# Kernel optimization log

Hardware: AMD Instinct MI355X
Metric: run time of the kernel (lower is better)

The kernel has to match this reference:

```python
import jax, jax.numpy as jnp
import numpy as np

D_MODEL = 1024
N_HEAD = 16
D_K = D_MODEL // N_HEAD
B, T = 4, 2048


def setup_inputs() -> dict:
    key = jax.random.key(0)
    ks = jax.random.split(key, 12)
    s = 1.0 / np.sqrt(D_MODEL)
    inp = {
        "q": jax.random.normal(ks[0], (B, T, D_MODEL), jnp.float32),
        "k": jax.random.normal(ks[1], (B, T, D_MODEL), jnp.float32),
        "v": jax.random.normal(ks[2], (B, T, D_MODEL), jnp.float32),
        # causal mask: True = allowed
        "mask": jnp.tril(jnp.ones((T, T), bool))[None, None, :, :],
        "w_q": jax.random.uniform(ks[3], (D_MODEL, D_MODEL), jnp.float32, -s, s),
        "b_q": jax.random.uniform(ks[4], (D_MODEL,), jnp.float32, -s, s),
        "w_k": jax.random.uniform(ks[5], (D_MODEL, D_MODEL), jnp.float32, -s, s),
        "b_k": jax.random.uniform(ks[6], (D_MODEL,), jnp.float32, -s, s),
        "w_v": jax.random.uniform(ks[7], (D_MODEL, D_MODEL), jnp.float32, -s, s),
        "b_v": jax.random.uniform(ks[8], (D_MODEL,), jnp.float32, -s, s),
        "w_o": jax.random.uniform(ks[9], (D_MODEL, D_MODEL), jnp.float32, -s, s),
        "b_o": jax.random.uniform(ks[10], (D_MODEL,), jnp.float32, -s, s),
    }
    return inp


def reference(q, k, v, mask, w_q, b_q, w_k, b_k, w_v, b_v, w_o, b_o):
    b, tq, d = q.shape
    tk = k.shape[1]
    # projections (torch Linear: x @ W^T + b)
    qh = (q @ w_q.T + b_q).reshape(b, tq, N_HEAD, D_K).transpose(0, 2, 1, 3)
    kh = (k @ w_k.T + b_k).reshape(b, tk, N_HEAD, D_K).transpose(0, 2, 1, 3)
    vh = (v @ w_v.T + b_v).reshape(b, tk, N_HEAD, D_K).transpose(0, 2, 1, 3)
    # scores: (b, h, tq, tk)
    scores = jnp.einsum("bhqd,bhkd->bhqk", qh, kh) / jnp.sqrt(jnp.float32(D_K))
    scores = jnp.where(mask, scores, jnp.finfo(scores.dtype).min)
    attn = jax.nn.softmax(scores, axis=-1)
    out = jnp.einsum("bhqk,bhkd->bhqd", attn, vh)
    out = out.transpose(0, 2, 1, 3).reshape(b, tq, d)
    return out @ w_o.T + b_o
```

## Files before the change

### kernel.cpp

```cpp
#include <hip/hip_runtime.h>

typedef unsigned short u16;
typedef __attribute__((ext_vector_type(8))) short bf16x8;
typedef __attribute__((ext_vector_type(4))) float f32x4;

#define D_MODEL 1024
#define T_SEQ   2048
#define NB      4
#define NH      16
#define DKH     64

__device__ __forceinline__ u16 f2bf(float x) {
  union { float f; unsigned u; } v; v.f = x;
  unsigned r = v.u + 0x7fffu + ((v.u >> 16) & 1u);
  return (u16)(r >> 16);
}
__device__ __forceinline__ unsigned pack2(float a, float b) {
  return (unsigned)f2bf(a) | ((unsigned)f2bf(b) << 16);
}
__device__ __forceinline__ float fexp2(float x) {
#if __has_builtin(__builtin_amdgcn_exp2f)
  return __builtin_amdgcn_exp2f(x);
#else
  return __expf(x * 0.6931471805599453f);
#endif
}

__device__ __forceinline__ void gload16(const void* g, void* l) {
  __builtin_amdgcn_global_load_lds(
      (const __attribute__((address_space(1))) unsigned*)g,
      (__attribute__((address_space(3))) unsigned*)l, 16, 0, 0);
}

__global__ void cast_w4(const float* __restrict__ s0, const float* __restrict__ s1,
                        const float* __restrict__ s2, const float* __restrict__ s3,
                        u16* __restrict__ o0, u16* __restrict__ o1,
                        u16* __restrict__ o2, u16* __restrict__ o3) {
  const int which = blockIdx.y;
  const float* s = which == 0 ? s0 : which == 1 ? s1 : which == 2 ? s2 : s3;
  u16* o = which == 0 ? o0 : which == 1 ? o1 : which == 2 ? o2 : o3;
  int i = ((int)blockIdx.x * 256 + (int)threadIdx.x) * 4;
  float4 v = *(const float4*)(s + i);
  uint2 u; u.x = pack2(v.x, v.y); u.y = pack2(v.z, v.w);
  *(uint2*)(o + i) = u;
}

__global__ __launch_bounds__(256) void gemm_qkv(
    const float* __restrict__ qin, const float* __restrict__ kin, const float* __restrict__ vin,
    const u16* __restrict__ wq, const u16* __restrict__ wk, const u16* __restrict__ wv,
    const float* __restrict__ bqp, const float* __restrict__ bkp, const float* __restrict__ bvp,
    u16* __restrict__ Xq, u16* __restrict__ Xk, u16* __restrict__ Xv) {
  const int z = blockIdx.z;
  const float* A = z == 0 ? qin : z == 1 ? kin : vin;
  const u16* W = z == 0 ? wq : z == 1 ? wk : wv;
  const float* bias = z == 0 ? bqp : z == 1 ? bkp : bvp;
  u16* C = z == 0 ? Xq : z == 1 ? Xk : Xv;
  const float osc = z == 0 ? 0.18033688011112042f : 1.0f;
  const int K = 1024, N = 1024;

  __shared__ __align__(16) u16 As[128 * 72];
  __shared__ __align__(16) u16 Bs[128 * 64];
  const int tid = threadIdx.x;
  const int w = tid >> 6, lane = tid & 63;
  const int wm = w & 1, wn = w >> 1;
  const int l15 = lane & 15, quad = lane >> 4;
  const int m0 = blockIdx.x * 128, n0 = blockIdx.y * 128;
  const int srow = tid >> 3;
  const int scol = (tid & 7) * 8;
  const int lrow = lane >> 3;
  const int lcol = ((lane & 7) ^ lrow) * 8;

  const u16* gB = W + (size_t)(n0 + w * 32 + lrow) * K + lcol;
  u16* lB = Bs + w * 32 * 64;

  f32x4 zero4 = {0.f, 0.f, 0.f, 0.f};
  f32x4 acc[4][4];
#pragma unroll
  for (int i = 0; i < 4; ++i)
#pragma unroll
    for (int j = 0; j < 4; ++j) acc[i][j] = zero4;

  for (int kb = 0; kb < K; kb += 64) {
    uint4 ra[4];
#pragma unroll
    for (int r = 0; r < 4; ++r) {
      const float* p = A + (size_t)(m0 + r * 32 + srow) * K + kb + scol;
      float4 x = *(const float4*)p;
      float4 y = *(const float4*)(p + 4);
      ra[r].x = pack2(x.x, x.y); ra[r].y = pack2(x.z, x.w);
      ra[r].z = pack2(y.x, y.y); ra[r].w = pack2(y.z, y.w);
    }
    __syncthreads();
#pragma unroll
    for (int t = 0; t < 4; ++t) gload16(gB + kb + t * 8 * K, lB + t * 512);
#pragma unroll
    for (int r = 0; r < 4; ++r)
      *(uint4*)(As + (r * 32 + srow) * 72 + scol) = ra[r];
    __syncthreads();

#pragma unroll
    for (int ks = 0; ks < 2; ++ks) {
      const int sB = (((ks * 4 + quad) ^ (l15 & 7)) * 8);
      bf16x8 af[4], bfr[4];
#pragma unroll
      for (int i = 0; i < 4; ++i)
        af[i] = *(const bf16x8*)(As + (wm * 64 + i * 16 + l15) * 72 + ks * 32 + quad * 8);
#pragma unroll
      for (int i = 0; i < 4; ++i)
        bfr[i] = *(const bf16x8*)(Bs + (wn * 64 + i * 16 + l15) * 64 + sB);
#pragma unroll
      for (int mi = 0; mi < 4; ++mi)
#pragma unroll
        for (int ni = 0; ni < 4; ++ni)
          acc[mi][ni] = __builtin_amdgcn_mfma_f32_16x16x32_bf16(af[mi], bfr[ni], acc[mi][ni], 0, 0, 0);
    }
  }

#pragma unroll
  for (int ni = 0; ni < 4; ++ni) {
    int col = n0 + wn * 64 + ni * 16 + l15;
    float bv = bias[col];
#pragma unroll
    for (int mi = 0; mi < 4; ++mi) {
      int row = m0 + wm * 64 + mi * 16 + quad * 4;
#pragma unroll
      for (int r = 0; r < 4; ++r)
        C[(size_t)(row + r) * N + col] = f2bf((acc[mi][ni][r] + bv) * osc);
    }
  }
}

__global__ __launch_bounds__(256) void gemm_nt_f32out(const u16* __restrict__ Ab,
                                                      const u16* __restrict__ W,
                                                      const float* __restrict__ bias,
                                                      float* __restrict__ Cp,
                                                      int M, int N, int K) {
  __shared__ __align__(16) u16 As[128 * 64];
  __shared__ __align__(16) u16 Bs[128 * 64];
  const int tid = threadIdx.x;
  const int w = tid >> 6, lane = tid & 63;
  const int wm = w & 1, wn = w >> 1;
  const int l15 = lane & 15, quad = lane >> 4;
  const int m0 = blockIdx.x * 128, n0 = blockIdx.y * 128;
  const int lrow = lane >> 3;
  const int lcol = ((lane & 7) ^ lrow) * 8;

  const u16* gA = Ab + (size_t)(m0 + w * 32 + lrow) * K + lcol;
  const u16* gB = W  + (size_t)(n0 + w * 32 + lrow) * K + lcol;
  u16* lA = As + w * 32 * 64;
  u16* lB = Bs + w * 32 * 64;

  f32x4 zero4 = {0.f, 0.f, 0.f, 0.f};
  f32x4 acc[4][4];
#pragma unroll
  for (int i = 0; i < 4; ++i)
#pragma unroll
    for (int j = 0; j < 4; ++j) acc[i][j] = zero4;

  for (int kb = 0; kb < K; kb += 64) {
    __syncthreads();
#pragma unroll
    for (int t = 0; t < 4; ++t) gload16(gA + kb + t * 8 * K, lA + t * 512);
#pragma unroll
    for (int t = 0; t < 4; ++t) gload16(gB + kb + t * 8 * K, lB + t * 512);
    __syncthreads();

#pragma unroll
    for (int ks = 0; ks < 2; ++ks) {
      const int sA = (((ks * 4 + quad) ^ (l15 & 7)) * 8);
      bf16x8 af[4], bfr[4];
#pragma unroll
      for (int i = 0; i < 4; ++i)
        af[i] = *(const bf16x8*)(As + (wm * 64 + i * 16 + l15) * 64 + sA);
#pragma unroll
      for (int i = 0; i < 4; ++i)
        bfr[i] = *(const bf16x8*)(Bs + (wn * 64 + i * 16 + l15) * 64 + sA);
#pragma unroll
      for (int mi = 0; mi < 4; ++mi)
#pragma unroll
        for (int ni = 0; ni < 4; ++ni)
          acc[mi][ni] = __builtin_amdgcn_mfma_f32_16x16x32_bf16(af[mi], bfr[ni], acc[mi][ni], 0, 0, 0);
    }
  }

#pragma unroll
  for (int ni = 0; ni < 4; ++ni) {
    int col = n0 + wn * 64 + ni * 16 + l15;
    float bv = bias[col];
#pragma unroll
    for (int mi = 0; mi < 4; ++mi) {
      int row = m0 + wm * 64 + mi * 16 + quad * 4;
#pragma unroll
      for (int r = 0; r < 4; ++r)
        Cp[(size_t)(row + r) * N + col] = acc[mi][ni][r] + bv;
    }
  }
}

__global__ __launch_bounds__(256) void attn_fwd(const u16* __restrict__ Xq,
                                                const u16* __restrict__ Xk,
                                                const u16* __restrict__ Xv,
                                                u16* __restrict__ O) {
  __shared__ __align__(16) u16 Kt[2][64 * 64];
  __shared__ __align__(16) u16 Vt[2][64 * 72];

  const int qt = 15 - (int)blockIdx.x;
  const int h = blockIdx.y, b = blockIdx.z;
  const int tid = threadIdx.x;
  const int w = tid >> 6, lane = tid & 63;
  const int l15 = lane & 15, quad = lane >> 4;
  const size_t base = (size_t)b * T_SEQ * D_MODEL;
  const int hd = h * DKH;
  const int q0 = qt * 128;
  const int rowb0 = q0 + w * 32;

  const int krow = lane >> 3;
  const int kcol = ((lane & 7) ^ krow) * 8;
  const u16* gK = Xk + base + (size_t)(w * 16 + krow) * D_MODEL + hd + kcol;

  const int vkey = lane, vdp = w;
  const int skey = (vkey & 0x20) | ((vkey & 0xC) << 1) | ((vkey & 0x10) >> 2) | (vkey & 3);
  const u16* gV = Xv + base + (size_t)vkey * D_MODEL + hd + vdp * 16;

  bf16x8 bq[2][2];
#pragma unroll
  for (int mi = 0; mi < 2; ++mi)
#pragma unroll
    for (int ks = 0; ks < 2; ++ks)
      bq[mi][ks] = *(const bf16x8*)(Xq + base + (size_t)(rowb0 + mi * 16 + l15) * D_MODEL
                                    + hd + ks * 32 + quad * 8);

  bf16x8 bones;
#pragma unroll
  for (int i = 0; i < 8; ++i) bones[i] = (short)0x3F80;

  f32x4 zero4 = {0.f, 0.f, 0.f, 0.f};
  f32x4 o[4][2], ol[2];
#pragma unroll
  for (int di = 0; di < 4; ++di)
#pragma unroll
    for (int mi = 0; mi < 2; ++mi) o[di][mi] = zero4;
#pragma unroll
  for (int mi = 0; mi < 2; ++mi) ol[mi] = zero4;

  const int nkt = 2 * qt + 2;

  gload16(gK, Kt[0] + (w * 16) * 64);
  gload16(gK + (size_t)8 * D_MODEL, Kt[0] + (w * 16 + 8) * 64);
  uint4 va0 = *(const uint4*)gV;
  uint4 va1 = *(const uint4*)(gV + 8);

  for (int kt = 0; kt < nkt; ++kt) {
    const int k0 = kt * 64;
    const int buf = kt & 1;

    {
      union { uint4 u; u16 hh[8]; } u0, u1;
      u0.u = va0; u1.u = va1;
      u16* vtb = Vt[buf];
#pragma unroll
      for (int i = 0; i < 8; ++i) {
        vtb[(vdp * 16 + i) * 72 + skey] = u0.hh[i];
        vtb[(vdp * 16 + 8 + i) * 72 + skey] = u1.hh[i];
      }
    }
    __syncthreads();

    if (kt + 1 < nkt) {
      const u16* gk2 = gK + (size_t)(k0 + 64) * D_MODEL;
      gload16(gk2, Kt[1 - buf] + (w * 16) * 64);
      gload16(gk2 + (size_t)8 * D_MODEL, Kt[1 - buf] + (w * 16 + 8) * 64);
      const u16* gv2 = gV + (size_t)(k0 + 64) * D_MODEL;
      va0 = *(const uint4*)gv2;
      va1 = *(const uint4*)(gv2 + 8);
    }

    f32x4 st[4][2];
#pragma unroll
    for (int ni = 0; ni < 4; ++ni) {
      const u16* kr = Kt[buf] + (ni * 16 + l15) * 64;
      bf16x8 a0 = *(const bf16x8*)(kr + ((quad ^ (l15 & 7)) * 8));
      bf16x8 a1 = *(const bf16x8*)(kr + (((4 + quad) ^ (l15 & 7)) * 8));
#pragma unroll
      for (int mi = 0; mi < 2; ++mi) {
        f32x4 t = zero4;
        t = __builtin_amdgcn_mfma_f32_16x16x32_bf16(a0, bq[mi][0], t, 0, 0, 0);
        t = __builtin_amdgcn_mfma_f32_16x16x32_bf16(a1, bq[mi][1], t, 0, 0, 0);
        st[ni][mi] = t;
      }
    }

    bf16x8 bp[2][2];
#pragma unroll
    for (int mi = 0; mi < 2; ++mi) {
      const int qa = rowb0 + mi * 16 + l15;
      if (k0 + 63 > rowb0 + mi * 16) {
#pragma unroll
        for (int ni = 0; ni < 4; ++ni)
#pragma unroll
          for (int r = 0; r < 4; ++r)
            if (k0 + ni * 16 + quad * 4 + r > qa) st[ni][mi][r] = -1e30f;
      }
      float p[4][4];
#pragma unroll
      for (int ni = 0; ni < 4; ++ni)
#pragma unroll
        for (int r = 0; r < 4; ++r)
          p[ni][r] = fexp2(st[ni][mi][r]);
#pragma unroll
      for (int js = 0; js < 2; ++js) {
        union { bf16x8 v; unsigned d[4]; } ub;
        ub.d[0] = pack2(p[2 * js][0], p[2 * js][1]);
        ub.d[1] = pack2(p[2 * js][2], p[2 * js][3]);
        ub.d[2] = pack2(p[2 * js + 1][0], p[2 * js + 1][1]);
        ub.d[3] = pack2(p[2 * js + 1][2], p[2 * js + 1][3]);
        bp[mi][js] = ub.v;
      }
    }

#pragma unroll
    for (int js = 0; js < 2; ++js) {
      bf16x8 av[4];
#pragma unroll
      for (int di = 0; di < 4; ++di)
        av[di] = *(const bf16x8*)(Vt[buf] + (di * 16 + l15) * 72 + js * 32 + quad * 8);
#pragma unroll
      for (int di = 0; di < 4; ++di)
#pragma unroll
        for (int mi = 0; mi < 2; ++mi)
          o[di][mi] = __builtin_amdgcn_mfma_f32_16x16x32_bf16(av[di], bp[mi][js], o[di][mi], 0, 0, 0);
#pragma unroll
      for (int mi = 0; mi < 2; ++mi)
        ol[mi] = __builtin_amdgcn_mfma_f32_16x16x32_bf16(bones, bp[mi][js], ol[mi], 0, 0, 0);
    }
  }

#pragma unroll
  for (int mi = 0; mi < 2; ++mi) {
    const float inv = 1.0f / ol[mi][0];
    const size_t qa = rowb0 + mi * 16 + l15;
#pragma unroll
    for (int di = 0; di < 4; ++di) {
      uint2 s2;
      s2.x = pack2(o[di][mi][0] * inv, o[di][mi][1] * inv);
      s2.y = pack2(o[di][mi][2] * inv, o[di][mi][3] * inv);
      *(uint2*)(O + base + qa * D_MODEL + hd + di * 16 + quad * 4) = s2;
    }
  }
}

extern "C" void kernel_launch(void* const* d_in, const int* in_sizes, int n_in,
                              void* d_out, int out_size, void* d_ws, size_t ws_size,
                              hipStream_t stream) {
  const float* q   = (const float*)d_in[0];
  const float* k   = (const float*)d_in[1];
  const float* v   = (const float*)d_in[2];
  const float* w_q = (const float*)d_in[4];  const float* b_q = (const float*)d_in[5];
  const float* w_k = (const float*)d_in[6];  const float* b_k = (const float*)d_in[7];
  const float* w_v = (const float*)d_in[8];  const float* b_v = (const float*)d_in[9];
  const float* w_o = (const float*)d_in[10]; const float* b_o = (const float*)d_in[11];

  u16* ws = (u16*)d_ws;
  const size_t NTD = (size_t)NB * T_SEQ * D_MODEL;
  const size_t WSZ = (size_t)D_MODEL * D_MODEL;
  u16* wqb = ws;
  u16* wkb = wqb + WSZ;
  u16* wvb = wkb + WSZ;
  u16* wob = wvb + WSZ;
  u16* Xq  = wob + WSZ;
  u16* Xk  = Xq + NTD;
  u16* Xv  = Xk + NTD;
  u16* Ob  = Xv + NTD;

  cast_w4<<<dim3(WSZ / 1024, 4), 256, 0, stream>>>(w_q, w_k, w_v, w_o, wqb, wkb, wvb, wob);

  gemm_qkv<<<dim3(64, 8, 3), 256, 0, stream>>>(q, k, v, wqb, wkb, wvb,
                                               b_q, b_k, b_v, Xq, Xk, Xv);

  attn_fwd<<<dim3(16, NH, NB), 256, 0, stream>>>(Xq, Xk, Xv, Ob);

  gemm_nt_f32out<<<dim3(64, 8), 256, 0, stream>>>(Ob, wob, b_o, (float*)d_out,
                                                  8192, 1024, 1024);
}
```

Measured before the change: 395.6 us.

## Pair causal query tiles per block, split keys across two wave halves, remap GEMM tiles

The attention kernel now runs 512 threads per block. Each block handles two query tiles (qt and 15-qt) so the causal work per block is balanced. The two 4-wave halves process the even and odd key tiles and merge their partial outputs and row sums through shared memory. V is stored in shared memory with an XOR swizzle instead of padding. The GEMMs use a 1D grid with an XCD-aware block-to-tile mapping meant to improve L2 locality, at the cost of extra synchronisation and shared-memory traffic in the merge.

```diff
diff --git a/kernel.cpp b/kernel.cpp
--- a/kernel.cpp
+++ b/kernel.cpp
@@ -43,6 +43,11 @@
   float4 v = *(const float4*)(s + i);
   uint2 u; u.x = pack2(v.x, v.y); u.y = pack2(v.z, v.w);
   *(uint2*)(o + i) = u;
+}
+
+__device__ __forceinline__ void xcd_decode(int bid, int& m0, int& n0) {
+  m0 = ((bid & 7) + ((bid >> 6) << 3)) << 7;
+  n0 = ((bid >> 3) & 7) << 7;
 }
 
 __global__ __launch_bounds__(256) void gemm_qkv(
@@ -64,7 +69,7 @@
   const int w = tid >> 6, lane = tid & 63;
   const int wm = w & 1, wn = w >> 1;
   const int l15 = lane & 15, quad = lane >> 4;
-  const int m0 = blockIdx.x * 128, n0 = blockIdx.y * 128;
+  int m0, n0; xcd_decode(blockIdx.x, m0, n0);
   const int srow = tid >> 3;
   const int scol = (tid & 7) * 8;
   const int lrow = lane >> 3;
@@ -141,7 +146,7 @@
   const int w = tid >> 6, lane = tid & 63;
   const int wm = w & 1, wn = w >> 1;
   const int l15 = lane & 15, quad = lane >> 4;
-  const int m0 = blockIdx.x * 128, n0 = blockIdx.y * 128;
+  int m0, n0; xcd_decode(blockIdx.x, m0, n0);
   const int lrow = lane >> 3;
   const int lcol = ((lane & 7) ^ lrow) * 8;
 
@@ -197,155 +202,210 @@
   }
 }
 
-__global__ __launch_bounds__(256) void attn_fwd(const u16* __restrict__ Xq,
-                                                const u16* __restrict__ Xk,
-                                                const u16* __restrict__ Xv,
-                                                u16* __restrict__ O) {
-  __shared__ __align__(16) u16 Kt[2][64 * 64];
-  __shared__ __align__(16) u16 Vt[2][64 * 72];
-
-  const int qt = 15 - (int)blockIdx.x;
+__global__ __launch_bounds__(512, 4) void attn_fwd(const u16* __restrict__ Xq,
+                                                   const u16* __restrict__ Xk,
+                                                   const u16* __restrict__ Xv,
+                                                   u16* __restrict__ O) {
+  __shared__ __align__(16) char smem[65536];
+
+  const int xp = blockIdx.x;
   const int h = blockIdx.y, b = blockIdx.z;
   const int tid = threadIdx.x;
   const int w = tid >> 6, lane = tid & 63;
+  const int half = w >> 2, wl = w & 3;
   const int l15 = lane & 15, quad = lane >> 4;
   const size_t base = (size_t)b * T_SEQ * D_MODEL;
   const int hd = h * DKH;
-  const int q0 = qt * 128;
-  const int rowb0 = q0 + w * 32;
+
+  u16* KtH = (u16*)(smem + half * 32768);
+  u16* VtH = (u16*)(smem + half * 32768 + 16384);
+  float* ML = (float*)(smem + 16384);
+  float* MO = (float*)(smem + 32768);
 
   const int krow = lane >> 3;
   const int kcol = ((lane & 7) ^ krow) * 8;
-  const u16* gK = Xk + base + (size_t)(w * 16 + krow) * D_MODEL + hd + kcol;
-
-  const int vkey = lane, vdp = w;
+  const u16* gK = Xk + base + (size_t)(wl * 16 + krow) * D_MODEL + hd + kcol;
+  const int vkey = lane;
   const int skey = (vkey & 0x20) | ((vkey & 0xC) << 1) | ((vkey & 0x10) >> 2) | (vkey & 3);
-  const u16* gV = Xv + base + (size_t)vkey * D_MODEL + hd + vdp * 16;
-
-  bf16x8 bq[2][2];
-#pragma unroll
-  for (int mi = 0; mi < 2; ++mi)
-#pragma unroll
-    for (int ks = 0; ks < 2; ++ks)
-      bq[mi][ks] = *(const bf16x8*)(Xq + base + (size_t)(rowb0 + mi * 16 + l15) * D_MODEL
-                                    + hd + ks * 32 + quad * 8);
+  const int scb = skey >> 3, sci = skey & 7;
+  const u16* gV = Xv + base + (size_t)vkey * D_MODEL + hd + wl * 16;
 
   bf16x8 bones;
 #pragma unroll
   for (int i = 0; i < 8; ++i) bones[i] = (short)0x3F80;
 
   f32x4 zero4 = {0.f, 0.f, 0.f, 0.f};
-  f32x4 o[4][2], ol[2];
-#pragma unroll
-  for (int di = 0; di < 4; ++di)
-#pragma unroll
-    for (int mi = 0; mi < 2; ++mi) o[di][mi] = zero4;
-#pragma unroll
-  for (int mi = 0; mi < 2; ++mi) ol[mi] = zero4;
-
-  const int nkt = 2 * qt + 2;
-
-  gload16(gK, Kt[0] + (w * 16) * 64);
-  gload16(gK + (size_t)8 * D_MODEL, Kt[0] + (w * 16 + 8) * 64);
-  uint4 va0 = *(const uint4*)gV;
-  uint4 va1 = *(const uint4*)(gV + 8);
-
-  for (int kt = 0; kt < nkt; ++kt) {
-    const int k0 = kt * 64;
-    const int buf = kt & 1;
-
-    {
-      union { uint4 u; u16 hh[8]; } u0, u1;
-      u0.u = va0; u1.u = va1;
-      u16* vtb = Vt[buf];
-#pragma unroll
-      for (int i = 0; i < 8; ++i) {
-        vtb[(vdp * 16 + i) * 72 + skey] = u0.hh[i];
-        vtb[(vdp * 16 + 8 + i) * 72 + skey] = u1.hh[i];
-      }
-    }
-    __syncthreads();
-
-    if (kt + 1 < nkt) {
-      const u16* gk2 = gK + (size_t)(k0 + 64) * D_MODEL;
-      gload16(gk2, Kt[1 - buf] + (w * 16) * 64);
-      gload16(gk2 + (size_t)8 * D_MODEL, Kt[1 - buf] + (w * 16 + 8) * 64);
-      const u16* gv2 = gV + (size_t)(k0 + 64) * D_MODEL;
-      va0 = *(const uint4*)gv2;
-      va1 = *(const uint4*)(gv2 + 8);
-    }
-
-    f32x4 st[4][2];
-#pragma unroll
-    for (int ni = 0; ni < 4; ++ni) {
-      const u16* kr = Kt[buf] + (ni * 16 + l15) * 64;
-      bf16x8 a0 = *(const bf16x8*)(kr + ((quad ^ (l15 & 7)) * 8));
-      bf16x8 a1 = *(const bf16x8*)(kr + (((4 + quad) ^ (l15 & 7)) * 8));
+  int tcnt = 0;
+
+  {
+    const u16* gk0 = gK + (size_t)(half * 64) * D_MODEL;
+    gload16(gk0, KtH + (wl * 16) * 64);
+    gload16(gk0 + (size_t)8 * D_MODEL, KtH + (wl * 16 + 8) * 64);
+  }
+  const u16* gv0 = gV + (size_t)(half * 64) * D_MODEL;
+  uint4 va0 = *(const uint4*)gv0;
+  uint4 va1 = *(const uint4*)(gv0 + 8);
+
+  for (int ph = 0; ph < 2; ++ph) {
+    const int qt = ph ? xp : 15 - xp;
+    const int q0 = qt << 7;
+    const int rowb0 = q0 + wl * 32;
+
+    bf16x8 bq[2][2];
+#pragma unroll
+    for (int mi = 0; mi < 2; ++mi)
+#pragma unroll
+      for (int ks = 0; ks < 2; ++ks)
+        bq[mi][ks] = *(const bf16x8*)(Xq + base + (size_t)(rowb0 + mi * 16 + l15) * D_MODEL
+                                      + hd + ks * 32 + quad * 8);
+
+    f32x4 o[4][2], ol[2];
+#pragma unroll
+    for (int di = 0; di < 4; ++di)
+#pragma unroll
+      for (int mi = 0; mi < 2; ++mi) o[di][mi] = zero4;
+#pragma unroll
+    for (int mi = 0; mi < 2; ++mi) ol[mi] = zero4;
+
+    const int cnt = qt + 1;
+
+    if (ph == 1 && half == 1) {
+      const int fb = tcnt & 1;
+      const u16* gk1 = gK + (size_t)64 * D_MODEL;
+      gload16(gk1, KtH + fb * 4096 + (wl * 16) * 64);
+      gload16(gk1 + (size_t)8 * D_MODEL, KtH + fb * 4096 + (wl * 16 + 8) * 64);
+    }
+
+    for (int i = 0; i < cnt; ++i, ++tcnt) {
+      const int k0 = (half + 2 * i) * 64;
+      const int buf = tcnt & 1;
+      u16* ktb = KtH + buf * 4096;
+      u16* vtb = VtH + buf * 4096;
+
+      {
+        union { uint4 u; u16 hh[8]; } u0, u1;
+        u0.u = va0; u1.u = va1;
+#pragma unroll
+        for (int ii = 0; ii < 8; ++ii) {
+          vtb[(wl * 16 + ii) * 64 + ((scb ^ ii) << 3) + sci] = u0.hh[ii];
+          vtb[(wl * 16 + 8 + ii) * 64 + ((scb ^ ii) << 3) + sci] = u1.hh[ii];
+        }
+      }
+      __syncthreads();
+
+      const bool inph = (i + 1 < cnt);
+      if (inph || ph == 0) {
+        const int k0n = inph ? k0 + 128 : half * 64;
+        if (inph || half == 0) {
+          const u16* gk2 = gK + (size_t)k0n * D_MODEL;
+          u16* ktn = KtH + (1 - buf) * 4096;
+          gload16(gk2, ktn + (wl * 16) * 64);
+          gload16(gk2 + (size_t)8 * D_MODEL, ktn + (wl * 16 + 8) * 64);
+        }
+        const u16* gv2 = gV + (size_t)k0n * D_MODEL;
+        va0 = *(const uint4*)gv2;
+        va1 = *(const uint4*)(gv2 + 8);
+      }
+
+      f32x4 st[4][2];
+#pragma unroll
+      for (int ni = 0; ni < 4; ++ni) {
+        const u16* kr = ktb + (ni * 16 + l15) * 64;
+        bf16x8 a0 = *(const bf16x8*)(kr + ((quad ^ (l15 & 7)) << 3));
+        bf16x8 a1 = *(const bf16x8*)(kr + (((4 + quad) ^ (l15 & 7)) << 3));
+#pragma unroll
+        for (int mi = 0; mi < 2; ++mi) {
+          f32x4 t = zero4;
+          t = __builtin_amdgcn_mfma_f32_16x16x32_bf16(a0, bq[mi][0], t, 0, 0, 0);
+          t = __builtin_amdgcn_mfma_f32_16x16x32_bf16(a1, bq[mi][1], t, 0, 0, 0);
+          st[ni][mi] = t;
+        }
+      }
+
+      bf16x8 bp[2][2];
 #pragma unroll
       for (int mi = 0; mi < 2; ++mi) {
-        f32x4 t = zero4;
-        t = __builtin_amdgcn_mfma_f32_16x16x32_bf16(a0, bq[mi][0], t, 0, 0, 0);
-        t = __builtin_amdgcn_mfma_f32_16x16x32_bf16(a1, bq[mi][1], t, 0, 0, 0);
-        st[ni][mi] = t;
-      }
-    }
-
-    bf16x8 bp[2][2];
-#pragma unroll
-    for (int mi = 0; mi < 2; ++mi) {
-      const int qa = rowb0 + mi * 16 + l15;
-      if (k0 + 63 > rowb0 + mi * 16) {
+        const int qa = rowb0 + mi * 16 + l15;
+        if (k0 + 63 > rowb0 + mi * 16) {
+#pragma unroll
+          for (int ni = 0; ni < 4; ++ni)
+#pragma unroll
+            for (int r = 0; r < 4; ++r)
+              if (k0 + ni * 16 + quad * 4 + r > qa) st[ni][mi][r] = -1e30f;
+        }
+        float p[4][4];
 #pragma unroll
         for (int ni = 0; ni < 4; ++ni)
 #pragma unroll
           for (int r = 0; r < 4; ++r)
-            if (k0 + ni * 16 + quad * 4 + r > qa) st[ni][mi][r] = -1e30f;
-      }
-      float p[4][4];
-#pragma unroll
-      for (int ni = 0; ni < 4; ++ni)
-#pragma unroll
-        for (int r = 0; r < 4; ++r)
-          p[ni][r] = fexp2(st[ni][mi][r]);
+            p[ni][r] = fexp2(st[ni][mi][r]);
+#pragma unroll
+        for (int js = 0; js < 2; ++js) {
+          union { bf16x8 v; unsigned d[4]; } ub;
+          ub.d[0] = pack2(p[2 * js][0], p[2 * js][1]);
+          ub.d[1] = pack2(p[2 * js][2], p[2 * js][3]);
+          ub.d[2] = pack2(p[2 * js + 1][0], p[2 * js + 1][1]);
+          ub.d[3] = pack2(p[2 * js + 1][2], p[2 * js + 1][3]);
+          bp[mi][js] = ub.v;
+        }
+      }
+
 #pragma unroll
       for (int js = 0; js < 2; ++js) {
-        union { bf16x8 v; unsigned d[4]; } ub;
-        ub.d[0] = pack2(p[2 * js][0], p[2 * js][1]);
-        ub.d[1] = pack2(p[2 * js][2], p[2 * js][3]);
-        ub.d[2] = pack2(p[2 * js + 1][0], p[2 * js + 1][1]);
-        ub.d[3] = pack2(p[2 * js + 1][2], p[2 * js + 1][3]);
-        bp[mi][js] = ub.v;
-      }
-    }
-
-#pragma unroll
-    for (int js = 0; js < 2; ++js) {
-      bf16x8 av[4];
-#pragma unroll
-      for (int di = 0; di < 4; ++di)
-        av[di] = *(const bf16x8*)(Vt[buf] + (di * 16 + l15) * 72 + js * 32 + quad * 8);
-#pragma unroll
-      for (int di = 0; di < 4; ++di)
+        bf16x8 av[4];
+#pragma unroll
+        for (int di = 0; di < 4; ++di)
+          av[di] = *(const bf16x8*)(vtb + (di * 16 + l15) * 64
+                                    + (((js * 4 + quad) ^ (l15 & 7)) << 3));
+#pragma unroll
+        for (int di = 0; di < 4; ++di)
+#pragma unroll
+          for (int mi = 0; mi < 2; ++mi)
+            o[di][mi] = __builtin_amdgcn_mfma_f32_16x16x32_bf16(av[di], bp[mi][js], o[di][mi], 0, 0, 0);
 #pragma unroll
         for (int mi = 0; mi < 2; ++mi)
-          o[di][mi] = __builtin_amdgcn_mfma_f32_16x16x32_bf16(av[di], bp[mi][js], o[di][mi], 0, 0, 0);
-#pragma unroll
-      for (int mi = 0; mi < 2; ++mi)
-        ol[mi] = __builtin_amdgcn_mfma_f32_16x16x32_bf16(bones, bp[mi][js], ol[mi], 0, 0, 0);
-    }
-  }
-
-#pragma unroll
-  for (int mi = 0; mi < 2; ++mi) {
-    const float inv = 1.0f / ol[mi][0];
-    const size_t qa = rowb0 + mi * 16 + l15;
-#pragma unroll
-    for (int di = 0; di < 4; ++di) {
-      uint2 s2;
-      s2.x = pack2(o[di][mi][0] * inv, o[di][mi][1] * inv);
-      s2.y = pack2(o[di][mi][2] * inv, o[di][mi][3] * inv);
-      *(uint2*)(O + base + qa * D_MODEL + hd + di * 16 + quad * 4) = s2;
-    }
+          ol[mi] = __builtin_amdgcn_mfma_f32_16x16x32_bf16(bones, bp[mi][js], ol[mi], 0, 0, 0);
+      }
+    }
+
+    __syncthreads();
+    if (half == 1) {
+#pragma unroll
+      for (int mi = 0; mi < 2; ++mi) {
+        const int ql = wl * 32 + mi * 16 + l15;
+        if (quad == 0) ML[ql] = ol[mi][0];
+#pragma unroll
+        for (int di = 0; di < 4; ++di)
+#pragma unroll
+          for (int r = 0; r < 4; ++r) {
+            const int d = di * 16 + quad * 4 + r;
+            MO[ql * 64 + (d ^ ((ql & 7) << 3))] = o[di][mi][r];
+          }
+      }
+    }
+    __syncthreads();
+    if (half == 0) {
+#pragma unroll
+      for (int mi = 0; mi < 2; ++mi) {
+        const int ql = wl * 32 + mi * 16 + l15;
+        const float inv = 1.0f / (ol[mi][0] + ML[ql]);
+        const size_t qa = q0 + ql;
+#pragma unroll
+        for (int di = 0; di < 4; ++di) {
+          float t[4];
+#pragma unroll
+          for (int r = 0; r < 4; ++r) {
+            const int d = di * 16 + quad * 4 + r;
+            t[r] = (o[di][mi][r] + MO[ql * 64 + (d ^ ((ql & 7) << 3))]) * inv;
+          }
+          uint2 s2;
+          s2.x = pack2(t[0], t[1]);
+          s2.y = pack2(t[2], t[3]);
+          *(uint2*)(O + base + qa * D_MODEL + hd + di * 16 + quad * 4) = s2;
+        }
+      }
+    }
+    __syncthreads();
   }
 }
 
@@ -374,11 +434,11 @@
 
   cast_w4<<<dim3(WSZ / 1024, 4), 256, 0, stream>>>(w_q, w_k, w_v, w_o, wqb, wkb, wvb, wob);
 
-  gemm_qkv<<<dim3(64, 8, 3), 256, 0, stream>>>(q, k, v, wqb, wkb, wvb,
-                                               b_q, b_k, b_v, Xq, Xk, Xv);
-
-  attn_fwd<<<dim3(16, NH, NB), 256, 0, stream>>>(Xq, Xk, Xv, Ob);
-
-  gemm_nt_f32out<<<dim3(64, 8), 256, 0, stream>>>(Ob, wob, b_o, (float*)d_out,
-                                                  8192, 1024, 1024);
-}
+  gemm_qkv<<<dim3(512, 1, 3), 256, 0, stream>>>(q, k, v, wqb, wkb, wvb,
+                                                b_q, b_k, b_v, Xq, Xk, Xv);
+
+  attn_fwd<<<dim3(8, NH, NB), 512, 0, stream>>>(Xq, Xk, Xv, Ob);
+
+  gemm_nt_f32out<<<dim3(512), 256, 0, stream>>>(Ob, wob, b_o, (float*)d_out,
+                                                8192, 1024, 1024);
+}
```

Result: slower. 438.3 us (+10.8%).
